# Kernel tuning notes

Hardware: AMD Instinct MI355X
Metric: run time of the kernel (lower is better)

The kernel has to match this reference:

```python
import jax, jax.numpy as jnp
import numpy as np

B, S, H = 8, 2048, 1024
NH, HD, NS, K = 16, 64, 64, 4  # num_heads, head_dim, state_size, conv kernel


def setup_inputs() -> dict:
    key = jax.random.key(0)
    ks = jax.random.split(key, 16)
    sc = 0.02
    return {
        "x": jax.random.normal(ks[0], (B, S, H), dtype=jnp.float32),
        # weights stored (in, out) so y = x @ W + b
        "in_proj_w": jax.random.normal(ks[1], (H, 2 * H), dtype=jnp.float32) * sc,
        "conv_w": jax.random.normal(ks[2], (H, 1, K), dtype=jnp.float32) * sc,
        "conv_b": jnp.zeros((H,), dtype=jnp.float32),
        "bb_w": jax.random.normal(ks[3], (HD, HD), dtype=jnp.float32) * sc,
        "bb_b": jnp.zeros((HD,), dtype=jnp.float32),
        "f1_w": jax.random.normal(ks[4], (HD, NS), dtype=jnp.float32) * sc,
        "f1_b": jnp.zeros((NS,), dtype=jnp.float32),
        "f2_w": jax.random.normal(ks[5], (HD, NS), dtype=jnp.float32) * sc,
        "f2_b": jnp.zeros((NS,), dtype=jnp.float32),
        "tau_a_w": jax.random.normal(ks[6], (HD, NS), dtype=jnp.float32) * sc,
        "tau_a_b": jnp.zeros((NS,), dtype=jnp.float32),
        "tau_b": jnp.zeros((NS,), dtype=jnp.float32),
        "decay_w": jax.random.normal(ks[7], (HD, NS), dtype=jnp.float32) * sc,
        "decay_b": jnp.zeros((NS,), dtype=jnp.float32),
        "state_out_w": jax.random.normal(ks[8], (NS, HD), dtype=jnp.float32) * sc,
        "state_out_b": jnp.zeros((HD,), dtype=jnp.float32),
        "out_proj_w": jax.random.normal(ks[9], (H, H), dtype=jnp.float32) * sc,
    }


def _short_conv(x, w, b):
    # x: (B,S,D) depthwise causal conv, kernel K, left-pad K-1
    xc = jnp.transpose(x, (0, 2, 1))  # (B,D,S)
    y = jax.lax.conv_general_dilated(
        xc, w, window_strides=(1,), padding=[(K - 1, 0)],
        feature_group_count=H, dimension_numbers=("NCH", "OIH", "NCH"))
    y = y + b[None, :, None]
    return jnp.transpose(y, (0, 2, 1))  # (B,S,D)


def _scan(decay, candidate):
    # decay, candidate: (B,S,NH,NS); h_t = d_t*h_{t-1} + (1-d_t)*c_t
    d = jnp.transpose(decay, (1, 0, 2, 3))      # (S,B,NH,NS)
    c = jnp.transpose(candidate, (1, 0, 2, 3))

    def step(h, dc):
        dt, ct = dc
        h = dt * h + (1.0 - dt) * ct
        return h, h

    h0 = jnp.zeros(d.shape[1:], dtype=decay.dtype)
    _, hs = jax.lax.scan(step, h0, (d, c))
    return jnp.transpose(hs, (1, 0, 2, 3))      # (B,S,NH,NS)


def reference(x, in_proj_w, conv_w, conv_b, bb_w, bb_b, f1_w, f1_b,
              f2_w, f2_b, tau_a_w, tau_a_b, tau_b, decay_w, decay_b,
              state_out_w, state_out_b, out_proj_w):
    xz = x @ in_proj_w                       # (B,S,2H)
    x_path, z_gate = jnp.split(xz, 2, axis=-1)
    x_path = jax.nn.silu(_short_conv(x_path, conv_w, conv_b))
    x_heads = x_path.reshape(B, S, NH, HD)
    bb = jax.nn.silu(x_heads @ bb_w + bb_b)  # backbone (1 layer)
    f1 = jnp.tanh(bb @ f1_w + f1_b)
    f2 = jnp.tanh(bb @ f2_w + f2_b)
    tau = jax.nn.sigmoid(bb @ tau_a_w + tau_a_b + tau_b)
    candidate = f1 * (1.0 - tau) + f2 * tau
    decay = jax.nn.sigmoid(bb @ decay_w + decay_b)
    h_seq = _scan(decay, candidate)          # (B,S,NH,NS)
    out = h_seq @ state_out_w + state_out_b  # (B,S,NH,HD)
    out = out.reshape(B, S, H)
    out = out * jax.nn.silu(z_gate)
    return out @ out_proj_w
```

## Files before the change

kernel.cpp:

```cpp
#include <hip/hip_runtime.h>
#include <hip/hip_bf16.h>
#include <math.h>

#define BN   8
#define SN   2048
#define HN   1024
#define NTOK 16384
#define NHD  16
#define HDD  64
#define NSD  64

typedef __attribute__((ext_vector_type(8))) short short8;
typedef __attribute__((ext_vector_type(4))) float f32x4;

__device__ __forceinline__ float fsig(float x)  { return 1.f / (1.f + __expf(-x)); }
__device__ __forceinline__ float fsilu(float x) { return x / (1.f + __expf(-x)); }
__device__ __forceinline__ float ftanh(float x) {
    const float t = __expf(-2.f * fabsf(x));
    const float r = (1.f - t) / (1.f + t);
    return x >= 0.f ? r : -r;
}
__device__ __forceinline__ unsigned pack_cd(float cand, float dec) {
    __hip_bfloat16 cb_ = __float2bfloat16(cand);
    __hip_bfloat16 db_ = __float2bfloat16(dec);
    return (unsigned)*(unsigned short*)&cb_ | ((unsigned)*(unsigned short*)&db_ << 16);
}
__device__ __forceinline__ float bf2f(unsigned short u) {
    return __uint_as_float((unsigned)u << 16);
}
__device__ __forceinline__ void gload_lds16(const void* g, void* l) {
    __builtin_amdgcn_global_load_lds(
        (const __attribute__((address_space(1))) unsigned int*)g,
        (__attribute__((address_space(3))) unsigned int*)l, 16, 0, 0);
}

__global__ __launch_bounds__(256)
void x_to_a_bf(const float* __restrict__ X, __hip_bfloat16* __restrict__ A)
{
    const int idx = blockIdx.x * 256 + threadIdx.x;
    const int r = idx >> 7;
    const int c = idx & 127;
    const float* src = &X[(size_t)r * 1024 + c * 8];
    alignas(16) __hip_bfloat16 b[8];
#pragma unroll
    for (int j = 0; j < 8; ++j) b[j] = __float2bfloat16(src[j]);
    const int cs = (c & ~3) | ((c & 3) ^ ((r >> 1) & 3));
    *(short8*)&A[(size_t)r * 1024 + cs * 8] = *(const short8*)b;
}

__global__ __launch_bounds__(256)
void w_to_bt_bf(const float* __restrict__ W, __hip_bfloat16* __restrict__ BT, int N)
{
    __shared__ float t[64][65];
    const int k0 = blockIdx.x * 64;
    const int n0 = blockIdx.y * 64;
    const int c  = threadIdx.x & 63, r4 = threadIdx.x >> 6;
#pragma unroll
    for (int rr = 0; rr < 64; rr += 4)
        t[rr + r4][c] = W[(size_t)(k0 + rr + r4) * N + n0 + c];
    __syncthreads();
#pragma unroll
    for (int oo = 0; oo < 2; ++oo) {
        const int o = r4 * 2 + oo;
        alignas(16) __hip_bfloat16 b[8];
#pragma unroll
        for (int j = 0; j < 8; ++j)
            b[j] = __float2bfloat16(t[o * 8 + j][c]);
        const int n = n0 + c;
        const int cglob = (k0 >> 3) + o;
        const int cs = (cglob & ~3) | ((cglob & 3) ^ ((n >> 1) & 3));
        *(short8*)&BT[(size_t)n * 1024 + cs * 8] = *(const short8*)b;
    }
}

__global__ __launch_bounds__(256)
void w5_to_wt(const float* __restrict__ w0, const float* __restrict__ w1,
              const float* __restrict__ w2, const float* __restrict__ w3,
              const float* __restrict__ w4, __hip_bfloat16* __restrict__ WT5)
{
    const int idx = blockIdx.x * 256 + threadIdx.x;
    if (idx >= 2560) return;
    const int o = idx & 7, n = (idx >> 3) & 63, mat = idx >> 9;
    const float* W = mat == 0 ? w0 : mat == 1 ? w1 : mat == 2 ? w2 : mat == 3 ? w3 : w4;
    alignas(16) __hip_bfloat16 b[8];
#pragma unroll
    for (int j = 0; j < 8; ++j)
        b[j] = __float2bfloat16(W[(o * 8 + j) * 64 + n]);
    *(short8*)&WT5[(size_t)(mat * 64 + n) * 64 + ((o ^ (n & 7)) * 8)] = *(const short8*)b;
}

template<int NCT, int MODE>
__global__ __launch_bounds__(512, 4)
void mfma_gemm(const __hip_bfloat16* __restrict__ A,
               const __hip_bfloat16* __restrict__ BT,
               float* __restrict__ outf,
               __hip_bfloat16* __restrict__ xb, __hip_bfloat16* __restrict__ zb)
{
    __shared__ __hip_bfloat16 lds[2][12288];
    const int tid  = threadIdx.x;
    const int lane = tid & 63, wave = tid >> 6;
    const int wr   = wave >> 2, wc = wave & 3;
    const int l15  = lane & 15, l4 = lane >> 4;

    const int nwg = gridDim.x;
    const int cpx = nwg >> 3;
    const int swz = (blockIdx.x & 7) * cpx + (blockIdx.x >> 3);
    const int mt = swz / NCT, nt = swz % NCT;
    const int row0 = mt * 128, col0 = nt * 256;

    const int s_c = tid & 3;
    const int s_r = tid >> 2;

    f32x4 acc[4][4];
#pragma unroll
    for (int m = 0; m < 4; ++m)
#pragma unroll
        for (int n = 0; n < 4; ++n) acc[m][n] = (f32x4)0.f;

#define STAGE(TT, BUF)                                                         \
    {                                                                          \
        const int kk_ = (TT) << 5;                                             \
        gload_lds16(&A[(size_t)(row0 + s_r) * 1024 + kk_ + s_c * 8],           \
                    &lds[BUF][s_r * 32 + s_c * 8]);                            \
        _Pragma("unroll")                                                      \
        for (int h_ = 0; h_ < 2; ++h_) {                                       \
            const int r_ = h_ * 128 + s_r;                                     \
            gload_lds16(&BT[(size_t)(col0 + r_) * 1024 + kk_ + s_c * 8],       \
                        &lds[BUF][4096 + r_ * 32 + s_c * 8]);                  \
        }                                                                      \
    }

    STAGE(0, 0)
    __syncthreads();

    for (int t = 0; t < 32; ++t) {
        const int cur = t & 1, nxt = cur ^ 1;
        if (t < 31) STAGE(t + 1, nxt)

        const int ch = (l4 ^ ((l15 >> 1) & 3)) * 8;
        short8 af[4], bf[4];
#pragma unroll
        for (int m = 0; m < 4; ++m)
            af[m] = *(const short8*)&lds[cur][(wr * 64 + m * 16 + l15) * 32 + ch];
#pragma unroll
        for (int n = 0; n < 4; ++n)
            bf[n] = *(const short8*)&lds[cur][4096 + (wc * 64 + n * 16 + l15) * 32 + ch];

        __builtin_amdgcn_s_setprio(1);
#pragma unroll
        for (int m = 0; m < 4; ++m)
#pragma unroll
            for (int n = 0; n < 4; ++n)
                acc[m][n] = __builtin_amdgcn_mfma_f32_16x16x32_bf16(af[m], bf[n], acc[m][n], 0, 0, 0);
        __builtin_amdgcn_s_setprio(0);

        __syncthreads();
    }
#undef STAGE

    const int orow = l4 * 4, ocol = l15;
#pragma unroll
    for (int m = 0; m < 4; ++m)
#pragma unroll
        for (int n = 0; n < 4; ++n) {
            const int c = col0 + wc * 64 + n * 16 + ocol;
#pragma unroll
            for (int q = 0; q < 4; ++q) {
                const int r = row0 + wr * 64 + m * 16 + orow + q;
                const float v = acc[m][n][q];
                if (MODE == 0) {
                    outf[(size_t)r * (NCT * 256) + c] = v;
                } else {
                    if (c < 1024) xb[(size_t)r * 1024 + c] = __float2bfloat16(v);
                    else          zb[(size_t)r * 1024 + (c - 1024)] = __float2bfloat16(fsilu(v));
                }
            }
        }
}

__global__ __launch_bounds__(512, 4)
void backbone_mfma(const __hip_bfloat16* __restrict__ xpath,
                   const float* __restrict__ cw, const float* __restrict__ cb,
                   const __hip_bfloat16* __restrict__ WT5,
                   const float* __restrict__ bbb,
                   const float* __restrict__ f1b, const float* __restrict__ f2b,
                   const float* __restrict__ taub, const float* __restrict__ taub2,
                   const float* __restrict__ decb,
                   unsigned* __restrict__ cd)
{
    __shared__ __hip_bfloat16 Wl[5 * 64 * 64];
    __shared__ __hip_bfloat16 Bb[128 * 64];
    const int tid  = threadIdx.x;
    const int lane = tid & 63, wave = tid >> 6;
    const int l15  = lane & 15, l4 = lane >> 4;
    const int e7   = l15 & 7;

#pragma unroll
    for (int r = 0; r < 5; ++r) {
        const int blk = r * 8 + wave;
        gload_lds16(WT5 + blk * 512 + lane * 8, Wl + blk * 512);
    }

    const int bt = blockIdx.x * 8 + wave;
    const int t  = bt & (SN - 1);
    short8 xa[2];
#pragma unroll
    for (int s = 0; s < 2; ++s) {
        const int cb0 = l15 * 64 + (s * 4 + l4) * 8;
        float acc[8];
#pragma unroll
        for (int j = 0; j < 8; ++j) acc[j] = cb[cb0 + j];
        float4 cwv[8];
#pragma unroll
        for (int j = 0; j < 8; ++j) cwv[j] = *(const float4*)&cw[(cb0 + j) * 4];
        const float* cwf = (const float*)cwv;
#pragma unroll
        for (int k = 0; k < 4; ++k) {
            if (t - 3 + k >= 0) {
                const short8 u = *(const short8*)&xpath[(size_t)(bt - 3 + k) * 1024 + cb0];
#pragma unroll
                for (int j = 0; j < 8; ++j)
                    acc[j] += cwf[j * 4 + k] * bf2f((unsigned short)u[j]);
            }
        }
        alignas(16) __hip_bfloat16 b[8];
#pragma unroll
        for (int j = 0; j < 8; ++j) b[j] = __float2bfloat16(fsilu(acc[j]));
        xa[s] = *(const short8*)b;
    }

    __syncthreads();

#pragma unroll
    for (int nt = 0; nt < 4; ++nt) {
        short8 wb[2];
#pragma unroll
        for (int s = 0; s < 2; ++s)
            wb[s] = *(const short8*)&Wl[(nt * 16 + l15) * 64 + (((s * 4 + l4) ^ e7) * 8)];
        f32x4 ac = (f32x4)0.f;
        ac = __builtin_amdgcn_mfma_f32_16x16x32_bf16(xa[0], wb[0], ac, 0, 0, 0);
        ac = __builtin_amdgcn_mfma_f32_16x16x32_bf16(xa[1], wb[1], ac, 0, 0, 0);
        const int col = nt * 16 + l15;
        const float bc = bbb[col];
#pragma unroll
        for (int q = 0; q < 4; ++q) {
            const int r15 = l4 * 4 + q;
            Bb[(wave * 16 + r15) * 64 + ((col >> 3) ^ (r15 & 7)) * 8 + (col & 7)] =
                __float2bfloat16(fsilu(ac[q] + bc));
        }
    }

    short8 ba[2];
#pragma unroll
    for (int s = 0; s < 2; ++s)
        ba[s] = *(const short8*)&Bb[(wave * 16 + l15) * 64 + (((s * 4 + l4) ^ e7) * 8)];

#pragma unroll
    for (int nt = 0; nt < 4; ++nt) {
        f32x4 a2[4];
#pragma unroll
        for (int m = 0; m < 4; ++m) a2[m] = (f32x4)0.f;

#pragma unroll
        for (int mat = 0; mat < 4; ++mat) {
            short8 w2[2];
#pragma unroll
            for (int s = 0; s < 2; ++s)
                w2[s] = *(const short8*)&Wl[((mat + 1) * 64 + nt * 16 + l15) * 64 + (((s * 4 + l4) ^ e7) * 8)];
            a2[mat] = __builtin_amdgcn_mfma_f32_16x16x32_bf16(ba[0], w2[0], a2[mat], 0, 0, 0);
            a2[mat] = __builtin_amdgcn_mfma_f32_16x16x32_bf16(ba[1], w2[1], a2[mat], 0, 0, 0);
        }

        const int col = nt * 16 + l15;
        const float b1 = f1b[col], b2 = f2b[col];
        const float b3 = taub[col] + taub2[col], b4 = decb[col];
        const size_t Rbase = (size_t)blockIdx.x * 128 + wave * 16;
#pragma unroll
        for (int q = 0; q < 4; ++q) {
            const size_t R = Rbase + l4 * 4 + q;
            const float f1v = ftanh(a2[0][q] + b1);
            const float f2v = ftanh(a2[1][q] + b2);
            const float tv  = fsig (a2[2][q] + b3);
            const float dv  = fsig (a2[3][q] + b4);
            cd[R * 64 + col] = pack_cd(f1v * (1.f - tv) + f2v * tv, dv);
        }
    }
}

__global__ __launch_bounds__(256)
void scan_compose(const unsigned* __restrict__ cd,
                  float* __restrict__ Ach, float* __restrict__ Bch)
{
    const int idx = blockIdx.x * 256 + threadIdx.x;
    const int p  = idx & 1023;
    const int rest = idx >> 10;
    const int ch = rest & 63, b = rest >> 6;
    float A = 1.f, Bv = 0.f;
    const size_t base = ((size_t)(b * SN + ch * 32) << 10) + p;
    for (int t = 0; t < 32; ++t) {
        const unsigned u = cd[base + ((size_t)t << 10)];
        const float c = __uint_as_float(u << 16);
        const float d = __uint_as_float(u & 0xffff0000u);
        A  *= d;
        Bv  = d * Bv + (1.f - d) * c;
    }
    Ach[(ch << 13) + (b << 10) + p] = A;
    Bch[(ch << 13) + (b << 10) + p] = Bv;
}

__global__ __launch_bounds__(256)
void scan_chunks(const float* __restrict__ Ach, const float* __restrict__ Bch,
                 float* __restrict__ hstart)
{
    const int q = blockIdx.x * 256 + threadIdx.x;
    float h = 0.f;
    for (int ch = 0; ch < 64; ++ch) {
        hstart[(ch << 13) + q] = h;
        h = Ach[(ch << 13) + q] * h + Bch[(ch << 13) + q];
    }
}

__global__ __launch_bounds__(256)
void scan_apply(const unsigned* __restrict__ cd,
                const float* __restrict__ hstart, __hip_bfloat16* __restrict__ Hhl)
{
    const int idx = blockIdx.x * 256 + threadIdx.x;
    const int p  = idx & 1023;
    const int rest = idx >> 10;
    const int ch = rest & 63, b = rest >> 6;
    const int nh = p >> 6, ns = p & 63;
    const int hpos = ((ns >> 3) ^ (nh & 7)) * 8 + (ns & 7);
    float h = hstart[(ch << 13) + (b << 10) + p];
    const int t0 = b * SN + ch * 32;
    const size_t base = ((size_t)t0 << 10) + p;
    for (int t = 0; t < 32; ++t) {
        const unsigned u = cd[base + ((size_t)t << 10)];
        const float c = __uint_as_float(u << 16);
        const float d = __uint_as_float(u & 0xffff0000u);
        h = d * h + (1.f - d) * c;
        Hhl[((size_t)(t0 + t) * 16 + nh) * 64 + hpos] = __float2bfloat16(h);
    }
}

__global__ __launch_bounds__(256, 4)
void stateout_mfma(const __hip_bfloat16* __restrict__ Hhl,
                   const float* __restrict__ sow, const float* __restrict__ sob,
                   const __hip_bfloat16* __restrict__ zs, __hip_bfloat16* __restrict__ gA)
{
    __shared__ __hip_bfloat16 Wl[64 * 64];
    __shared__ __hip_bfloat16 Hl[128 * 64];
    const int tid  = threadIdx.x;
    const int lane = tid & 63, wave = tid >> 6;
    const int l15  = lane & 15, l4 = lane >> 4;
    const int e7   = l15 & 7;

    {
        const int n = tid & 63;
        const int o0 = tid >> 6;
#pragma unroll
        for (int oo = 0; oo < 2; ++oo) {
            const int o = o0 + oo * 4;
            alignas(16) __hip_bfloat16 b[8];
#pragma unroll
            for (int j = 0; j < 8; ++j)
                b[j] = __float2bfloat16(sow[(o * 8 + j) * 64 + n]);
            *(short8*)&Wl[n * 64 + ((o ^ (n & 7)) * 8)] = *(const short8*)b;
        }
    }
    const __hip_bfloat16* hsrc = Hhl + (size_t)blockIdx.x * 8192;
#pragma unroll
    for (int r = 0; r < 4; ++r) {
        const int blk = r * 4 + wave;
        gload_lds16(hsrc + blk * 512 + lane * 8, Hl + blk * 512);
    }
    __syncthreads();

    short8 ha[2][2];
#pragma unroll
    for (int mt2 = 0; mt2 < 2; ++mt2)
#pragma unroll
        for (int s = 0; s < 2; ++s)
            ha[mt2][s] = *(const short8*)&Hl[(wave * 32 + mt2 * 16 + l15) * 64 + (((s * 4 + l4) ^ e7) * 8)];

#pragma unroll
    for (int nt = 0; nt < 4; ++nt) {
        short8 wb[2];
#pragma unroll
        for (int s = 0; s < 2; ++s)
            wb[s] = *(const short8*)&Wl[(nt * 16 + l15) * 64 + (((s * 4 + l4) ^ e7) * 8)];
        f32x4 ac[2] = {(f32x4)0.f, (f32x4)0.f};
#pragma unroll
        for (int mt2 = 0; mt2 < 2; ++mt2) {
            ac[mt2] = __builtin_amdgcn_mfma_f32_16x16x32_bf16(ha[mt2][0], wb[0], ac[mt2], 0, 0, 0);
            ac[mt2] = __builtin_amdgcn_mfma_f32_16x16x32_bf16(ha[mt2][1], wb[1], ac[mt2], 0, 0, 0);
        }
        const int col = nt * 16 + l15;
        const float bj = sob[col];
#pragma unroll
        for (int mt2 = 0; mt2 < 2; ++mt2)
#pragma unroll
            for (int q = 0; q < 4; ++q) {
                const size_t th = (size_t)blockIdx.x * 128 + wave * 32 + mt2 * 16 + l4 * 4 + q;
                const float z = bf2f(*(const unsigned short*)&zs[th * 64 + col]);
                const float v = (ac[mt2][q] + bj) * z;
                const size_t token = th >> 4;
                const int colg = (int)(th & 15) * 64 + col;
                const int cg = colg >> 3, jg = colg & 7;
                const int cs = (cg & ~3) | ((cg & 3) ^ ((int)((token >> 1) & 3)));
                gA[token * 1024 + cs * 8 + jg] = __float2bfloat16(v);
            }
    }
}

extern "C" void kernel_launch(void* const* d_in, const int* in_sizes, int n_in,
                              void* d_out, int out_size, void* d_ws, size_t ws_size,
                              hipStream_t stream)
{
    const float* x     = (const float*)d_in[0];
    const float* ipw   = (const float*)d_in[1];
    const float* cw    = (const float*)d_in[2];
    const float* cb    = (const float*)d_in[3];
    const float* bbw   = (const float*)d_in[4];
    const float* bbb   = (const float*)d_in[5];
    const float* f1w   = (const float*)d_in[6];
    const float* f1b   = (const float*)d_in[7];
    const float* f2w   = (const float*)d_in[8];
    const float* f2b   = (const float*)d_in[9];
    const float* tauw  = (const float*)d_in[10];
    const float* taub  = (const float*)d_in[11];
    const float* taub2 = (const float*)d_in[12];
    const float* decw  = (const float*)d_in[13];
    const float* decb  = (const float*)d_in[14];
    const float* sow   = (const float*)d_in[15];
    const float* sob   = (const float*)d_in[16];
    const float* opw   = (const float*)d_in[17];

    float* out = (float*)d_out;
    char*  ws  = (char*)d_ws;
    const size_t MB = 1024 * 1024;

    __hip_bfloat16* Abf   = (__hip_bfloat16*)(ws);
    __hip_bfloat16* Hhl   = (__hip_bfloat16*)(ws + 32 * MB);
    __hip_bfloat16* xpath = (__hip_bfloat16*)(ws + 64 * MB);
    __hip_bfloat16* gA    = (__hip_bfloat16*)(ws + 64 * MB);
    __hip_bfloat16* BTin  = (__hip_bfloat16*)(ws + 128 * MB);
    unsigned*       cd    = (unsigned*)(ws + 128 * MB);
    __hip_bfloat16* WT5   = (__hip_bfloat16*)(ws + 192 * MB);
    float*          Ach   = (float*)(ws + 192 * MB);
    float*          Bch   = Ach + 524288;
    float*          hst   = Bch + 524288;
    __hip_bfloat16* BTout = (__hip_bfloat16*)(ws + 192 * MB);
    __hip_bfloat16* zsilu = (__hip_bfloat16*)out;

    x_to_a_bf<<<8192, 256, 0, stream>>>(x, Abf);
    w_to_bt_bf<<<dim3(16, 32), 256, 0, stream>>>(ipw, BTin, 2048);
    w5_to_wt<<<10, 256, 0, stream>>>(bbw, f1w, f2w, tauw, decw, WT5);
    mfma_gemm<8, 1><<<1024, 512, 0, stream>>>(Abf, BTin, nullptr, xpath, zsilu);
    backbone_mfma<<<2048, 512, 0, stream>>>(xpath, cw, cb, WT5, bbb, f1b, f2b,
                                            taub, taub2, decb, cd);
    scan_compose<<<2048, 256, 0, stream>>>(cd, Ach, Bch);
    scan_chunks<<<32, 256, 0, stream>>>(Ach, Bch, hst);
    scan_apply<<<2048, 256, 0, stream>>>(cd, hst, Hhl);
    w_to_bt_bf<<<dim3(16, 16), 256, 0, stream>>>(opw, BTout, 1024);
    stateout_mfma<<<2048, 256, 0, stream>>>(Hhl, sow, sob, zsilu, gA);
    mfma_gemm<4, 0><<<512, 512, 0, stream>>>(gA, BTout, out, nullptr, nullptr);
}
```

Measured before the change: 304.1 us.

## Fuse chunked scan apply into state-out MFMA kernel via LDS

Merges scan_apply and stateout_mfma into one kernel. Each 512-thread block replays one 32-token chunk of the scan straight into shared memory, then runs the state-out projection and z-gating from there. This removes the global write and re-read of the bf16 hidden-state buffer and one kernel launch. In exchange each block uses more LDS (about 72KB), which may lower occupancy, and each thread runs the serial scan for two state positions.

After: 312.0 us. +2.6%, slower.

```diff
diff --git a/kernel.cpp b/kernel.cpp
--- a/kernel.cpp
+++ b/kernel.cpp
@@ -320,67 +320,57 @@
     }
 }
 
-__global__ __launch_bounds__(256)
-void scan_apply(const unsigned* __restrict__ cd,
-                const float* __restrict__ hstart, __hip_bfloat16* __restrict__ Hhl)
-{
-    const int idx = blockIdx.x * 256 + threadIdx.x;
-    const int p  = idx & 1023;
-    const int rest = idx >> 10;
-    const int ch = rest & 63, b = rest >> 6;
-    const int nh = p >> 6, ns = p & 63;
-    const int hpos = ((ns >> 3) ^ (nh & 7)) * 8 + (ns & 7);
-    float h = hstart[(ch << 13) + (b << 10) + p];
-    const int t0 = b * SN + ch * 32;
-    const size_t base = ((size_t)t0 << 10) + p;
-    for (int t = 0; t < 32; ++t) {
-        const unsigned u = cd[base + ((size_t)t << 10)];
-        const float c = __uint_as_float(u << 16);
-        const float d = __uint_as_float(u & 0xffff0000u);
-        h = d * h + (1.f - d) * c;
-        Hhl[((size_t)(t0 + t) * 16 + nh) * 64 + hpos] = __float2bfloat16(h);
-    }
-}
-
-__global__ __launch_bounds__(256, 4)
-void stateout_mfma(const __hip_bfloat16* __restrict__ Hhl,
+__global__ __launch_bounds__(512, 4)
+void scanout_fused(const unsigned* __restrict__ cd,
+                   const float* __restrict__ hstart,
                    const float* __restrict__ sow, const float* __restrict__ sob,
-                   const __hip_bfloat16* __restrict__ zs, __hip_bfloat16* __restrict__ gA)
+                   const __hip_bfloat16* __restrict__ zs,
+                   __hip_bfloat16* __restrict__ gA)
 {
     __shared__ __hip_bfloat16 Wl[64 * 64];
-    __shared__ __hip_bfloat16 Hl[128 * 64];
+    __shared__ __hip_bfloat16 Hl[512 * 64];
     const int tid  = threadIdx.x;
     const int lane = tid & 63, wave = tid >> 6;
     const int l15  = lane & 15, l4 = lane >> 4;
     const int e7   = l15 & 7;
+    const int b  = blockIdx.x >> 6;
+    const int chk = blockIdx.x & 63;
 
     {
         const int n = tid & 63;
-        const int o0 = tid >> 6;
-#pragma unroll
-        for (int oo = 0; oo < 2; ++oo) {
-            const int o = o0 + oo * 4;
-            alignas(16) __hip_bfloat16 b[8];
-#pragma unroll
-            for (int j = 0; j < 8; ++j)
-                b[j] = __float2bfloat16(sow[(o * 8 + j) * 64 + n]);
-            *(short8*)&Wl[n * 64 + ((o ^ (n & 7)) * 8)] = *(const short8*)b;
-        }
-    }
-    const __hip_bfloat16* hsrc = Hhl + (size_t)blockIdx.x * 8192;
-#pragma unroll
-    for (int r = 0; r < 4; ++r) {
-        const int blk = r * 4 + wave;
-        gload_lds16(hsrc + blk * 512 + lane * 8, Hl + blk * 512);
+        const int o = tid >> 6;
+        alignas(16) __hip_bfloat16 bw[8];
+#pragma unroll
+        for (int j = 0; j < 8; ++j)
+            bw[j] = __float2bfloat16(sow[(o * 8 + j) * 64 + n]);
+        *(short8*)&Wl[n * 64 + ((o ^ (n & 7)) * 8)] = *(const short8*)bw;
+    }
+
+    const float* hs0 = hstart + (chk << 13) + (b << 10);
+    const int t0 = b * SN + chk * 32;
+#pragma unroll
+    for (int cp = 0; cp < 2; ++cp) {
+        const int p = tid + cp * 512;
+        const int nh = p >> 6, ns = p & 63;
+        const int hpos = ((ns >> 3) ^ (nh & 7)) * 8 + (ns & 7);
+        float h = hs0[p];
+        const size_t base = ((size_t)t0 << 10) + p;
+        for (int t = 0; t < 32; ++t) {
+            const unsigned u = cd[base + ((size_t)t << 10)];
+            const float c = __uint_as_float(u << 16);
+            const float d = __uint_as_float(u & 0xffff0000u);
+            h = d * h + (1.f - d) * c;
+            Hl[(t * 16 + nh) * 64 + hpos] = __float2bfloat16(h);
+        }
     }
     __syncthreads();
 
-    short8 ha[2][2];
-#pragma unroll
-    for (int mt2 = 0; mt2 < 2; ++mt2)
+    short8 ha[4][2];
+#pragma unroll
+    for (int mt = 0; mt < 4; ++mt)
 #pragma unroll
         for (int s = 0; s < 2; ++s)
-            ha[mt2][s] = *(const short8*)&Hl[(wave * 32 + mt2 * 16 + l15) * 64 + (((s * 4 + l4) ^ e7) * 8)];
+            ha[mt][s] = *(const short8*)&Hl[(wave * 64 + mt * 16 + l15) * 64 + (((s * 4 + l4) ^ e7) * 8)];
 
 #pragma unroll
     for (int nt = 0; nt < 4; ++nt) {
@@ -388,23 +378,26 @@
 #pragma unroll
         for (int s = 0; s < 2; ++s)
             wb[s] = *(const short8*)&Wl[(nt * 16 + l15) * 64 + (((s * 4 + l4) ^ e7) * 8)];
-        f32x4 ac[2] = {(f32x4)0.f, (f32x4)0.f};
-#pragma unroll
-        for (int mt2 = 0; mt2 < 2; ++mt2) {
-            ac[mt2] = __builtin_amdgcn_mfma_f32_16x16x32_bf16(ha[mt2][0], wb[0], ac[mt2], 0, 0, 0);
-            ac[mt2] = __builtin_amdgcn_mfma_f32_16x16x32_bf16(ha[mt2][1], wb[1], ac[mt2], 0, 0, 0);
+        f32x4 ac[4];
+#pragma unroll
+        for (int mt = 0; mt < 4; ++mt) ac[mt] = (f32x4)0.f;
+#pragma unroll
+        for (int mt = 0; mt < 4; ++mt) {
+            ac[mt] = __builtin_amdgcn_mfma_f32_16x16x32_bf16(ha[mt][0], wb[0], ac[mt], 0, 0, 0);
+            ac[mt] = __builtin_amdgcn_mfma_f32_16x16x32_bf16(ha[mt][1], wb[1], ac[mt], 0, 0, 0);
         }
         const int col = nt * 16 + l15;
         const float bj = sob[col];
 #pragma unroll
-        for (int mt2 = 0; mt2 < 2; ++mt2)
+        for (int mt = 0; mt < 4; ++mt)
 #pragma unroll
             for (int q = 0; q < 4; ++q) {
-                const size_t th = (size_t)blockIdx.x * 128 + wave * 32 + mt2 * 16 + l4 * 4 + q;
-                const float z = bf2f(*(const unsigned short*)&zs[th * 64 + col]);
-                const float v = (ac[mt2][q] + bj) * z;
-                const size_t token = th >> 4;
-                const int colg = (int)(th & 15) * 64 + col;
+                const int rloc  = wave * 64 + mt * 16 + l4 * 4 + q;
+                const int tokl  = rloc >> 4, nh = rloc & 15;
+                const size_t token = (size_t)t0 + tokl;
+                const float z = bf2f(*(const unsigned short*)&zs[token * 1024 + nh * 64 + col]);
+                const float v = (ac[mt][q] + bj) * z;
+                const int colg = nh * 64 + col;
                 const int cg = colg >> 3, jg = colg & 7;
                 const int cs = (cg & ~3) | ((cg & 3) ^ ((int)((token >> 1) & 3)));
                 gA[token * 1024 + cs * 8 + jg] = __float2bfloat16(v);
@@ -440,7 +433,6 @@
     const size_t MB = 1024 * 1024;
 
     __hip_bfloat16* Abf   = (__hip_bfloat16*)(ws);
-    __hip_bfloat16* Hhl   = (__hip_bfloat16*)(ws + 32 * MB);
     __hip_bfloat16* xpath = (__hip_bfloat16*)(ws + 64 * MB);
     __hip_bfloat16* gA    = (__hip_bfloat16*)(ws + 64 * MB);
     __hip_bfloat16* BTin  = (__hip_bfloat16*)(ws + 128 * MB);
@@ -460,8 +452,7 @@
                                             taub, taub2, decb, cd);
     scan_compose<<<2048, 256, 0, stream>>>(cd, Ach, Bch);
     scan_chunks<<<32, 256, 0, stream>>>(Ach, Bch, hst);
-    scan_apply<<<2048, 256, 0, stream>>>(cd, hst, Hhl);
     w_to_bt_bf<<<dim3(16, 16), 256, 0, stream>>>(opw, BTout, 1024);
-    stateout_mfma<<<2048, 256, 0, stream>>>(Hhl, sow, sob, zsilu, gA);
+    scanout_fused<<<512, 512, 0, stream>>>(cd, hst, sow, sob, zsilu, gA);
     mfma_gemm<4, 0><<<512, 512, 0, stream>>>(gA, BTout, out, nullptr, nullptr);
 }
```
